# Performance work log

Hardware: AMD Instinct MI355X
Metric: run time of the kernel (lower is better)

The kernel has to match this reference:

```python
import jax, jax.numpy as jnp
import numpy as np

B, D, S, SE, H, DFF = 4, 1024, 1024, 1024, 16, 4096
DH = D // H
NUDGE = 1e-7


def norm(x):
    # x: [B, D, S]; custom layer norm: mean over (1,2), then divide by full L2 norm
    size = x.shape[1] * x.shape[2]
    mean = jnp.sum(x, axis=(1, 2)) / size
    x = x - mean[:, None, None]
    std = jnp.sqrt(jnp.sum(x * x, axis=(1, 2)))
    return x / (std[:, None, None] + NUDGE)


def mha(q_in, kv_in, Wq, Wk, Wv, Wo, causal):
    # q_in: [B, Sq, D], kv_in: [B, Sk, D]
    Bq, Sq, _ = q_in.shape
    Sk = kv_in.shape[1]
    q = (q_in @ Wq).reshape(Bq, Sq, H, DH)
    k = (kv_in @ Wk).reshape(Bq, Sk, H, DH)
    v = (kv_in @ Wv).reshape(Bq, Sk, H, DH)
    scores = jnp.einsum('bqhd,bkhd->bhqk', q, k) / jnp.sqrt(jnp.asarray(DH, q.dtype))
    if causal:
        mask = jnp.tril(jnp.ones((Sq, Sk), dtype=bool))
        scores = jnp.where(mask, scores, jnp.finfo(scores.dtype).min)
    attn = jax.nn.softmax(scores, axis=-1)
    out = jnp.einsum('bhqk,bkhd->bqhd', attn, v).reshape(Bq, Sq, D)
    return out @ Wo


def setup_inputs() -> dict:
    key = jax.random.key(0)
    ks = jax.random.split(key, 13)
    w = lambda k, sh: jax.random.normal(k, sh, dtype=jnp.float32) * 0.02
    return {
        'embedding': jax.random.normal(ks[0], (B, D, SE), dtype=jnp.float32),
        'other_inputs': jax.random.normal(ks[1], (B, D, S), dtype=jnp.float32),
        'Wq_s': w(ks[2], (D, D)), 'Wk_s': w(ks[3], (D, D)),
        'Wv_s': w(ks[4], (D, D)), 'Wo_s': w(ks[5], (D, D)),
        'Wq_c': w(ks[6], (D, D)), 'Wk_c': w(ks[7], (D, D)),
        'Wv_c': w(ks[8], (D, D)), 'Wo_c': w(ks[9], (D, D)),
        'W1': w(ks[10], (D, DFF)), 'b1': jnp.zeros((DFF,), jnp.float32),
        'W2': w(ks[11], (DFF, D)), 'b2': jnp.zeros((D,), jnp.float32),
    }


def reference(embedding, other_inputs, Wq_s, Wk_s, Wv_s, Wo_s,
              Wq_c, Wk_c, Wv_c, Wo_c, W1, b1, W2, b2):
    # tensors are [B, D, S]; attention operates on [B, S, D]
    x = other_inputs.transpose(0, 2, 1)
    sa = mha(x, x, Wq_s, Wk_s, Wv_s, Wo_s, causal=True)
    post_attention = norm(other_inputs + sa.transpose(0, 2, 1))

    pa = post_attention.transpose(0, 2, 1)
    emb = embedding.transpose(0, 2, 1)
    ca = mha(pa, emb, Wq_c, Wk_c, Wv_c, Wo_c, causal=False)
    post_embedding = norm(post_attention + ca.transpose(0, 2, 1))

    # per-token MLP (original loops over axis 2 and restacks; here fully batched)
    pe = post_embedding.transpose(0, 2, 1)  # [B, S, D]
    ff = jax.nn.relu(pe @ W1 + b1) @ W2 + b2
    return norm(post_embedding + ff.transpose(0, 2, 1))
```

## Files before the change

### kernel.cpp

```cpp
#include <hip/hip_runtime.h>
#include <cmath>

#define B_   4
#define D_   1024
#define S_   1024
#define H_   16
#define DH_  64
#define DFF_ 4096

typedef __attribute__((ext_vector_type(8))) short bf16x8;
typedef __attribute__((ext_vector_type(4))) float f32x4;

__device__ __forceinline__ unsigned short f2b(float f) {
    unsigned int u = __float_as_uint(f);
    u += 0x7fffu + ((u >> 16) & 1u);
    return (unsigned short)(u >> 16);
}

__device__ __forceinline__ void gload_lds16(const unsigned short* g, unsigned short* l) {
    __builtin_amdgcn_global_load_lds(
        (const __attribute__((address_space(1))) void*)g,
        (__attribute__((address_space(3))) void*)l, 16, 0, 0);
}

template <int BM, int BN, bool RES>
__global__ __launch_bounds__(256, 2)
void gemm_t(const unsigned short* __restrict__ A,
            const unsigned short* __restrict__ Wt,
            const float* __restrict__ bias,
            const float* __restrict__ residual,
            float* __restrict__ Cf, unsigned short* __restrict__ Cb,
            float* __restrict__ partial,
            int N, int K, int lda, int ldb, long csplit, int relu)
{
    constexpr int FM = BM / 32, FN = BN / 32;
    __shared__ unsigned short As[BM * 64];
    __shared__ unsigned short Bs[BN * 64];
    const int tid = threadIdx.x;
    const int w = tid >> 6, lane = tid & 63;
    const int quad = lane >> 4, l16 = lane & 15;
    const int m0 = blockIdx.x * BM, n0 = blockIdx.y * BN;
    const int wm = (w >> 1) * (BM / 2), wn = (w & 1) * (BN / 2);
    const int srow = lane >> 3;
    const int scol = ((lane & 7) ^ srow) * 8;

    A  += (size_t)blockIdx.z * K;
    Wt += (size_t)blockIdx.z * K;
    if (Cf) Cf += (size_t)blockIdx.z * csplit;

    f32x4 acc[FM][FN] = {};

    for (int k0 = 0; k0 < K; k0 += 64) {
#pragma unroll
        for (int i = 0; i < BM / 32; ++i) {
            const int inst = w + 4 * i;
            gload_lds16(A + (size_t)(m0 + inst * 8 + srow) * lda + k0 + scol,
                        As + inst * 512);
        }
#pragma unroll
        for (int i = 0; i < BN / 32; ++i) {
            const int inst = w + 4 * i;
            gload_lds16(Wt + (size_t)(n0 + inst * 8 + srow) * ldb + k0 + scol,
                        Bs + inst * 512);
        }
        __syncthreads();

#pragma unroll
        for (int kk = 0; kk < 2; ++kk) {
            bf16x8 af[FM], bfr[FN];
#pragma unroll
            for (int i = 0; i < FM; ++i) {
                const int r = wm + i * 16 + l16;
                af[i] = *(const bf16x8*)&As[r * 64 + (((kk * 4 + quad) ^ (r & 7)) * 8)];
            }
#pragma unroll
            for (int j = 0; j < FN; ++j) {
                const int r = wn + j * 16 + l16;
                bfr[j] = *(const bf16x8*)&Bs[r * 64 + (((kk * 4 + quad) ^ (r & 7)) * 8)];
            }
#pragma unroll
            for (int i = 0; i < FM; ++i)
#pragma unroll
                for (int j = 0; j < FN; ++j)
                    acc[i][j] = __builtin_amdgcn_mfma_f32_16x16x32_bf16(af[i], bfr[j], acc[i][j], 0, 0, 0);
        }
        __syncthreads();
    }

    float s = 0.f, ss = 0.f;
#pragma unroll
    for (int i = 0; i < FM; ++i) {
        const int grow = m0 + wm + i * 16 + quad * 4;
#pragma unroll
        for (int j = 0; j < FN; ++j) {
            const int gcol = n0 + wn + j * 16 + l16;
            const float bv = bias ? bias[gcol] : 0.f;
#pragma unroll
            for (int r = 0; r < 4; ++r) {
                float vv = acc[i][j][r] + bv;
                if (relu) vv = fmaxf(vv, 0.f);
                if constexpr (RES) {
                    vv += residual[(size_t)(grow + r) * N + gcol];
                    s += vv; ss += vv * vv;
                    Cf[(size_t)(grow + r) * N + gcol] = vv;
                } else {
                    if (Cf) Cf[(size_t)(grow + r) * N + gcol] = vv;
                    if (Cb) Cb[(size_t)(grow + r) * N + gcol] = f2b(vv);
                }
            }
        }
    }

    if constexpr (RES) {
        float* rs = (float*)As;
        float* rss = rs + 256;
        rs[tid] = s; rss[tid] = ss;
        __syncthreads();
        for (int off = 128; off > 0; off >>= 1) {
            if (tid < off) { rs[tid] += rs[tid + off]; rss[tid] += rss[tid + off]; }
            __syncthreads();
        }
        if (tid == 0) {
            constexpr int YPB = S_ / BM;
            const int b = blockIdx.x / YPB;
            const int chunk = (blockIdx.x % YPB) * gridDim.y + blockIdx.y;
            const int chunks = YPB * gridDim.y;
            partial[((size_t)b * chunks + chunk) * 2 + 0] = rs[0];
            partial[((size_t)b * chunks + chunk) * 2 + 1] = rss[0];
        }
    }
}

__global__ void reduce2_res(const float* __restrict__ pc, const float* __restrict__ res,
                            const float* __restrict__ bias, float* __restrict__ y,
                            float* __restrict__ partial)
{
    const size_t pcs = (size_t)4096 * 1024;
    const int b = blockIdx.y;
    const size_t base = (size_t)b * 1048576 + (size_t)blockIdx.x * 16384;
    float s = 0.f, ss = 0.f;
    for (int i = threadIdx.x; i < 4096; i += 256) {
        const size_t e = base + (size_t)i * 4;
        float4 v0 = *(const float4*)&pc[e];
        float4 v1 = *(const float4*)&pc[e + pcs];
        float4 rv = *(const float4*)&res[e];
        float4 bv = *(const float4*)&bias[e & 1023];
        float4 o;
        o.x = v0.x + v1.x + rv.x + bv.x;
        o.y = v0.y + v1.y + rv.y + bv.y;
        o.z = v0.z + v1.z + rv.z + bv.z;
        o.w = v0.w + v1.w + rv.w + bv.w;
        *(float4*)&y[e] = o;
        s += o.x + o.y + o.z + o.w;
        ss += o.x * o.x + o.y * o.y + o.z * o.z + o.w * o.w;
    }
    __shared__ float rs[256], rss[256];
    rs[threadIdx.x] = s; rss[threadIdx.x] = ss;
    __syncthreads();
    for (int off = 128; off > 0; off >>= 1) {
        if (threadIdx.x < off) {
            rs[threadIdx.x] += rs[threadIdx.x + off];
            rss[threadIdx.x] += rss[threadIdx.x + off];
        }
        __syncthreads();
    }
    if (threadIdx.x == 0) {
        partial[((size_t)b * 64 + blockIdx.x) * 2 + 0] = rs[0];
        partial[((size_t)b * 64 + blockIdx.x) * 2 + 1] = rss[0];
    }
}

__device__ __forceinline__ void stats_reduce(const float* __restrict__ partial,
                                             int b, int chunks, int tid,
                                             float* rs, float* rss,
                                             float& mean, float& inv)
{
    float s = 0.f, ss = 0.f;
    for (int i = tid; i < chunks; i += 256) {
        s  += partial[((size_t)b * chunks + i) * 2 + 0];
        ss += partial[((size_t)b * chunks + i) * 2 + 1];
    }
    rs[tid] = s; rss[tid] = ss;
    __syncthreads();
    for (int off = 128; off > 0; off >>= 1) {
        if (tid < off) { rs[tid] += rs[tid + off]; rss[tid] += rss[tid + off]; }
        __syncthreads();
    }
    const float size = (float)(D_ * S_);
    const float m = rs[0] / size;
    const float var = fmaxf(rss[0] - size * m * m, 0.f);
    mean = m;
    inv = 1.f / (sqrtf(var) + 1e-7f);
    __syncthreads();
}

__global__ void norm_apply_dual(float* __restrict__ y, unsigned short* __restrict__ yb,
                                const float* __restrict__ partial, int chunks)
{
    __shared__ float rs[256], rss[256];
    const int b = blockIdx.y;
    float mean, inv;
    stats_reduce(partial, b, chunks, threadIdx.x, rs, rss, mean, inv);

    const int perBatch = D_ * S_;
    float4* y4 = (float4*)(y + (size_t)b * perBatch);
    unsigned short* yb_ = yb + (size_t)b * perBatch;
    const int n4 = perBatch / 4;
    for (int i = blockIdx.x * blockDim.x + threadIdx.x; i < n4;
         i += gridDim.x * blockDim.x) {
        float4 v = y4[i];
        v.x = (v.x - mean) * inv; v.y = (v.y - mean) * inv;
        v.z = (v.z - mean) * inv; v.w = (v.w - mean) * inv;
        y4[i] = v;
        ushort4 hh; hh.x = f2b(v.x); hh.y = f2b(v.y); hh.z = f2b(v.z); hh.w = f2b(v.w);
        *(ushort4*)(yb_ + (size_t)i * 4) = hh;
    }
}

template <bool CAUSAL>
__global__ __launch_bounds__(512, 4)
void attn_mfma3(const unsigned short* __restrict__ q, const unsigned short* __restrict__ k,
                const unsigned short* __restrict__ vt, unsigned short* __restrict__ o,
                int qstride, int kstride)
{
    __shared__ unsigned short Ks[128 * 64];
    __shared__ unsigned short Vt[64 * 128];
    __shared__ unsigned short Ps[8][16][72];
    const int tid = threadIdx.x;
    const int w = tid >> 6, lane = tid & 63;
    const int quad = lane >> 4, l16 = lane & 15;
    const int h = blockIdx.y, b = blockIdx.z;
    const int qt = CAUSAL ? ((blockIdx.x + h) & 7) : blockIdx.x;
    const int q0 = qt * 128;
    const int row0 = q0 + w * 16;

    const int ksr = lane >> 3, ksc = ((lane & 7) ^ (lane >> 3)) * 8;
    const int vsr = lane >> 4, vsc = lane & 15;

    const unsigned short* qA = q + (size_t)(b * S_ + row0 + l16) * qstride + h * DH_;
    const bf16x8 qa0 = *(const bf16x8*)(qA + quad * 8);
    const bf16x8 qa1 = *(const bf16x8*)(qA + 32 + quad * 8);

    f32x4 OA[4] = {};
    float lA[4] = {};

    const int nit = CAUSAL ? (qt + 1) : (S_ / 128);
    for (int t = 0; t < nit; ++t) {
        const int j0 = t * 128;
#pragma unroll
        for (int i = 0; i < 2; ++i) {
            const int ins = w + 8 * i;
            gload_lds16(k + (size_t)(b * S_ + j0 + ins * 8 + ksr) * kstride + h * DH_ + ksc,
                        Ks + ins * 512);
            const int vrow = ins * 4 + vsr;
            gload_lds16(vt + (size_t)((b * H_ + h) * DH_ + vrow) * S_ + j0
                           + ((vsc ^ (vrow & 15)) * 8),
                        Vt + ins * 512);
        }
        __syncthreads();

#pragma unroll
        for (int g = 0; g < 2; ++g) {
            const int jg = j0 + g * 64;
            const bool doW = !CAUSAL || (jg <= row0 + 15);
            const bool needMask = CAUSAL && doW && (jg + 63 > row0);

            if (doW) {
                f32x4 stA[4];
#pragma unroll
                for (int n = 0; n < 4; ++n) {
                    const int kr = g * 64 + n * 16 + l16;
                    const bf16x8 kf0 = *(const bf16x8*)&Ks[kr * 64 + ((quad ^ (kr & 7)) * 8)];
                    const bf16x8 kf1 = *(const bf16x8*)&Ks[kr * 64 + (((quad + 4) ^ (kr & 7)) * 8)];
                    f32x4 c = {};
                    c = __builtin_amdgcn_mfma_f32_16x16x32_bf16(qa0, kf0, c, 0, 0, 0);
                    c = __builtin_amdgcn_mfma_f32_16x16x32_bf16(qa1, kf1, c, 0, 0, 0);
                    stA[n] = c;
                }

#pragma unroll
                for (int n = 0; n < 4; ++n)
#pragma unroll
                    for (int r = 0; r < 4; ++r) {
                        float sv = stA[n][r] * 0.125f;
                        if (needMask) {
                            const int row = row0 + quad * 4 + r;
                            const int key = jg + n * 16 + l16;
                            if (key > row) sv = -1e30f;
                        }
                        const float p = __expf(sv);
                        lA[r] += p;
                        Ps[w][quad * 4 + r][n * 16 + l16] = f2b(p);
                    }
                __threadfence_block();

                const bf16x8 pa0 = *(const bf16x8*)&Ps[w][l16][quad * 8];
                const bf16x8 pa1 = *(const bf16x8*)&Ps[w][l16][32 + quad * 8];
#pragma unroll
                for (int n = 0; n < 4; ++n) {
                    const int vr = n * 16 + l16;
                    const bf16x8 vf0 = *(const bf16x8*)&Vt[vr * 128 + (((g * 8 + quad) ^ l16) * 8)];
                    const bf16x8 vf1 = *(const bf16x8*)&Vt[vr * 128 + (((g * 8 + quad + 4) ^ l16) * 8)];
                    OA[n] = __builtin_amdgcn_mfma_f32_16x16x32_bf16(pa0, vf0, OA[n], 0, 0, 0);
                    OA[n] = __builtin_amdgcn_mfma_f32_16x16x32_bf16(pa1, vf1, OA[n], 0, 0, 0);
                }
            }
        }
        __syncthreads();
    }

#pragma unroll
    for (int r = 0; r < 4; ++r) {
        float la = lA[r];
        la += __shfl_xor(la, 1); la += __shfl_xor(la, 2);
        la += __shfl_xor(la, 4); la += __shfl_xor(la, 8);
        const float ia = 1.f / la;
        const size_t baseA = (size_t)(b * S_ + row0 + quad * 4 + r) * D_ + h * DH_;
#pragma unroll
        for (int n = 0; n < 4; ++n)
            o[baseA + n * 16 + l16] = f2b(OA[n][r] * ia);
    }
}

__global__ void transpose_v(const unsigned short* __restrict__ src,
                            unsigned short* __restrict__ dst, int istride)
{
    __shared__ unsigned short t[32][34];
    const int z = blockIdx.z, b = z >> 4, h = z & 15;
    const int s0 = blockIdx.x * 32, d0 = blockIdx.y * 32;
    const int tx = threadIdx.x, ty = threadIdx.y;
#pragma unroll
    for (int i = 0; i < 4; ++i)
        t[ty + i * 8][tx] =
            src[(size_t)(b * S_ + s0 + ty + i * 8) * istride + h * DH_ + d0 + tx];
    __syncthreads();
#pragma unroll
    for (int i = 0; i < 4; ++i)
        dst[(size_t)(z * DH_ + d0 + ty + i * 8) * S_ + s0 + tx] = t[tx][ty + i * 8];
}

struct WJob { const float* src; int sld; long doff; int dld; };
struct WJobs { WJob j[16]; };

__global__ void wtrans_all(WJobs js, unsigned short* __restrict__ dst)
{
    __shared__ float tile[32][33];
    const WJob J = js.j[blockIdx.z];
    const int c0 = blockIdx.x * 32, r0 = blockIdx.y * 32;
    const int tx = threadIdx.x, ty = threadIdx.y;
#pragma unroll
    for (int i = 0; i < 4; ++i)
        tile[ty + i * 8][tx] = J.src[(size_t)(r0 + ty + i * 8) * J.sld + c0 + tx];
    __syncthreads();
#pragma unroll
    for (int i = 0; i < 4; ++i)
        dst[J.doff + (size_t)(c0 + ty + i * 8) * J.dld + r0 + tx] =
            f2b(tile[tx][ty + i * 8]);
}

__global__ void transpose_in(const float* __restrict__ other, const float* __restrict__ emb,
                             float* __restrict__ f0, unsigned short* __restrict__ xb,
                             unsigned short* __restrict__ eb)
{
    __shared__ float tile[32][33];
    const int z = blockIdx.z;
    const int b = z & 3;
    const bool isEmb = z >= 4;
    const float* ip = (isEmb ? emb : other) + (size_t)b * 1048576;
    const int c0 = blockIdx.x * 32, r0 = blockIdx.y * 32;
    const int tx = threadIdx.x, ty = threadIdx.y;
#pragma unroll
    for (int i = 0; i < 4; ++i)
        tile[ty + i * 8][tx] = ip[(size_t)(r0 + ty + i * 8) * 1024 + c0 + tx];
    __syncthreads();
#pragma unroll
    for (int i = 0; i < 4; ++i) {
        const float v = tile[tx][ty + i * 8];
        const size_t oidx = (size_t)b * 1048576 + (size_t)(c0 + ty + i * 8) * 1024 + r0 + tx;
        if (isEmb) eb[oidx] = f2b(v);
        else { f0[oidx] = v; xb[oidx] = f2b(v); }
    }
}

__global__ void transpose_out(const float* __restrict__ in, float* __restrict__ outf,
                              const float* __restrict__ partial, int chunks)
{
    __shared__ float tile[32][33];
    __shared__ float rs[256], rss[256];
    const int z = blockIdx.z;
    const int tx = threadIdx.x, ty = threadIdx.y;
    const int tid = ty * 32 + tx;

    float mean, inv;
    stats_reduce(partial, z, chunks, tid, rs, rss, mean, inv);

    const float* ip = in + (size_t)z * 1048576;
    const int c0 = blockIdx.x * 32, r0 = blockIdx.y * 32;
#pragma unroll
    for (int i = 0; i < 4; ++i)
        tile[ty + i * 8][tx] = ip[(size_t)(r0 + ty + i * 8) * 1024 + c0 + tx];
    __syncthreads();
#pragma unroll
    for (int i = 0; i < 4; ++i) {
        const float v = (tile[tx][ty + i * 8] - mean) * inv;
        outf[(size_t)z * 1048576 + (size_t)(c0 + ty + i * 8) * 1024 + r0 + tx] = v;
    }
}

extern "C" void kernel_launch(void* const* d_in, const int* in_sizes, int n_in,
                              void* d_out, int out_size, void* d_ws, size_t ws_size,
                              hipStream_t stream)
{
    const float* embedding = (const float*)d_in[0];
    const float* other     = (const float*)d_in[1];
    const float* W1 = (const float*)d_in[10];
    const float* b1 = (const float*)d_in[11];
    const float* W2 = (const float*)d_in[12];
    const float* b2 = (const float*)d_in[13];
    float* out = (float*)d_out;

    char* wsb = (char*)d_ws;
    const size_t MB = 1u << 20;
    float* f0 = (float*)(wsb + 0 * MB);
    float* f2 = (float*)(wsb + 16 * MB);
    unsigned short* wts  = (unsigned short*)(wsb + 32 * MB);
    unsigned short* wqkv = wts;
    unsigned short* wo_s = wts + 3 * 1048576;
    unsigned short* wq_c = wts + 4 * 1048576;
    unsigned short* wkv_c= wts + 5 * 1048576;
    unsigned short* wo_c = wts + 7 * 1048576;
    unsigned short* w1t  = wts + 8 * 1048576;
    unsigned short* w2t  = wts + 12 * 1048576;
    unsigned short* actA = (unsigned short*)(wsb + 64 * MB);
    unsigned short* actB = (unsigned short*)(wsb + 72 * MB);
    unsigned short* actC = (unsigned short*)(wsb + 80 * MB);
    unsigned short* actC2 = actC + 4 * 1048576;
    unsigned short* aout  = actC + 12 * 1048576;
    float* pc      = (float*)(wsb + 112 * MB);
    float* partial = (float*)(wsb + 176 * MB);

    const dim3 blkT(32, 8), blk256(256), blk512(512);
    const dim3 gAttn(S_ / 128, H_, B_);
    const dim3 gVt(32, 2, B_ * H_);
    const dim3 gApply(64, B_);

    WJobs js;
    for (int z = 0; z < 8; ++z)
        js.j[z] = { (const float*)d_in[2 + z], 1024, (long)z * 1048576, 1024 };
    for (int q = 0; q < 4; ++q)
        js.j[8 + q] = { W1 + (size_t)q * 1024, 4096, (long)(8 + q) * 1048576, 1024 };
    for (int q = 0; q < 4; ++q)
        js.j[12 + q] = { W2 + (size_t)q * 1048576, 1024, 12L * 1048576 + q * 1024, 4096 };
    hipLaunchKernelGGL(wtrans_all, dim3(32, 32, 16), blkT, 0, stream, js, wts);

    hipLaunchKernelGGL(transpose_in, dim3(32, 32, 8), blkT, 0, stream,
                       other, embedding, f0, actA, actB);

    hipLaunchKernelGGL((gemm_t<128, 128, false>), dim3(32, 24), blk256, 0, stream,
                       actA, wqkv, nullptr, nullptr, nullptr, actC, nullptr,
                       3072, 1024, 1024, 1024, 0L, 0);
    hipLaunchKernelGGL(transpose_v, gVt, blkT, 0, stream, actC + 2048, actA, 3072);
    hipLaunchKernelGGL(attn_mfma3<true>, gAttn, blk512, 0, stream,
                       actC, actC + 1024, actA, aout, 3072, 3072);
    hipLaunchKernelGGL((gemm_t<64, 128, true>), dim3(64, 8), blk256, 0, stream,
                       aout, wo_s, nullptr, f0, f2, nullptr, partial,
                       1024, 1024, 1024, 1024, 0L, 0);
    hipLaunchKernelGGL(norm_apply_dual, gApply, blk256, 0, stream, f2, actA, partial, 128);

    hipLaunchKernelGGL((gemm_t<64, 128, false>), dim3(64, 8), blk256, 0, stream,
                       actA, wq_c, nullptr, nullptr, nullptr, actC, nullptr,
                       1024, 1024, 1024, 1024, 0L, 0);
    hipLaunchKernelGGL((gemm_t<128, 128, false>), dim3(32, 16), blk256, 0, stream,
                       actB, wkv_c, nullptr, nullptr, nullptr, actC2, nullptr,
                       2048, 1024, 1024, 1024, 0L, 0);
    hipLaunchKernelGGL(transpose_v, gVt, blkT, 0, stream, actC2 + 1024, actB, 2048);
    hipLaunchKernelGGL(attn_mfma3<false>, gAttn, blk512, 0, stream,
                       actC, actC2, actB, aout, 1024, 2048);
    hipLaunchKernelGGL((gemm_t<64, 128, true>), dim3(64, 8), blk256, 0, stream,
                       aout, wo_c, nullptr, f2, f0, nullptr, partial,
                       1024, 1024, 1024, 1024, 0L, 0);
    hipLaunchKernelGGL(norm_apply_dual, gApply, blk256, 0, stream, f0, actA, partial, 128);

    hipLaunchKernelGGL((gemm_t<128, 128, false>), dim3(32, 32), blk256, 0, stream,
                       actA, w1t, b1, nullptr, nullptr, actC, nullptr,
                       DFF_, 1024, 1024, 1024, 0L, 1);
    hipLaunchKernelGGL((gemm_t<128, 128, false>), dim3(32, 8, 2), blk256, 0, stream,
                       actC, w2t, nullptr, nullptr, pc, nullptr, nullptr,
                       1024, 2048, 4096, 4096, (long)4096 * 1024, 0);
    hipLaunchKernelGGL(reduce2_res, gApply, blk256, 0, stream, pc, f0, b2, f2, partial);
    hipLaunchKernelGGL(transpose_out, dim3(32, 32, B_), blkT, 0, stream, f2, out, partial, 64);

    (void)in_sizes; (void)n_in; (void)out_size; (void)ws_size;
}
```

Before: 467.7 us.

## Add 512-thread 256-row GEMM kernel with double-buffered LDS for big projections

```diff
diff --git a/kernel.cpp b/kernel.cpp
--- a/kernel.cpp
+++ b/kernel.cpp
@@ -21,6 +21,114 @@
     __builtin_amdgcn_global_load_lds(
         (const __attribute__((address_space(1))) void*)g,
         (__attribute__((address_space(3))) void*)l, 16, 0, 0);
+}
+
+template <int BN>
+__global__ __launch_bounds__(512, 2)
+void gemm8(const unsigned short* __restrict__ A,
+           const unsigned short* __restrict__ Wt,
+           const float* __restrict__ bias,
+           float* __restrict__ Cf, unsigned short* __restrict__ Cb,
+           int N, int K, int lda, int ldb, long csplit, int relu)
+{
+    constexpr int BM = 256;
+    constexpr int FM = 8, FN = BN / 64;
+    constexpr int ACALLS = BM / 64, BCALLS = BN / 64;
+    constexpr int L = ACALLS + BCALLS;
+    constexpr int ASZ = BM * 64, BSZ = BN * 64;
+    __shared__ unsigned short lds[2 * (ASZ + BSZ)];
+
+    const int tid = threadIdx.x;
+    const int w = tid >> 6, lane = tid & 63;
+    const int quad = lane >> 4, l16 = lane & 15;
+    const int m0 = blockIdx.x * BM, n0 = blockIdx.y * BN;
+    const int wm = (w >> 2) * 128;
+    const int wn = (w & 3) * (BN / 4);
+    const int srow = lane >> 3;
+    const int scol = ((lane & 7) ^ srow) * 8;
+
+    A  += (size_t)blockIdx.z * K;
+    Wt += (size_t)blockIdx.z * K;
+    if (Cf) Cf += (size_t)blockIdx.z * csplit;
+
+    const int nt = K >> 6;
+
+    auto STAGE = [&](int t, int buf) {
+        const int k0 = t << 6;
+        unsigned short* As = lds + buf * (ASZ + BSZ);
+        unsigned short* Bs = As + ASZ;
+#pragma unroll
+        for (int i = 0; i < ACALLS; ++i) {
+            const int inst = w + 8 * i;
+            gload_lds16(A + (size_t)(m0 + inst * 8 + srow) * lda + k0 + scol,
+                        As + inst * 512);
+        }
+#pragma unroll
+        for (int i = 0; i < BCALLS; ++i) {
+            const int inst = w + 8 * i;
+            gload_lds16(Wt + (size_t)(n0 + inst * 8 + srow) * ldb + k0 + scol,
+                        Bs + inst * 512);
+        }
+    };
+
+    f32x4 acc[FM][FN] = {};
+
+    STAGE(0, 0);
+    STAGE(1, 1);
+    asm volatile("s_waitcnt vmcnt(%0)\n\ts_barrier" :: "i"(L) : "memory");
+
+    int cur = 0;
+    for (int t = 0; t < nt; ++t) {
+        const unsigned short* As = lds + cur * (ASZ + BSZ);
+        const unsigned short* Bs = As + ASZ;
+#pragma unroll
+        for (int kk = 0; kk < 2; ++kk) {
+            bf16x8 af[FM], bfr[FN];
+#pragma unroll
+            for (int i = 0; i < FM; ++i) {
+                const int r = wm + i * 16 + l16;
+                af[i] = *(const bf16x8*)&As[r * 64 + (((kk * 4 + quad) ^ (r & 7)) * 8)];
+            }
+#pragma unroll
+            for (int j = 0; j < FN; ++j) {
+                const int r = wn + j * 16 + l16;
+                bfr[j] = *(const bf16x8*)&Bs[r * 64 + (((kk * 4 + quad) ^ (r & 7)) * 8)];
+            }
+            __builtin_amdgcn_s_setprio(1);
+#pragma unroll
+            for (int i = 0; i < FM; ++i)
+#pragma unroll
+                for (int j = 0; j < FN; ++j)
+                    acc[i][j] = __builtin_amdgcn_mfma_f32_16x16x32_bf16(af[i], bfr[j], acc[i][j], 0, 0, 0);
+            __builtin_amdgcn_s_setprio(0);
+        }
+        if (t == nt - 1) break;
+        asm volatile("s_barrier" ::: "memory");
+        if (t + 2 < nt) {
+            STAGE(t + 2, cur);
+            asm volatile("s_waitcnt vmcnt(%0)\n\ts_barrier" :: "i"(L) : "memory");
+        } else {
+            asm volatile("s_waitcnt vmcnt(0)\n\ts_barrier" ::: "memory");
+        }
+        cur ^= 1;
+    }
+
+#pragma unroll
+    for (int i = 0; i < FM; ++i) {
+        const int grow = m0 + wm + i * 16 + quad * 4;
+#pragma unroll
+        for (int j = 0; j < FN; ++j) {
+            const int gcol = n0 + wn + j * 16 + l16;
+            const float bv = bias ? bias[gcol] : 0.f;
+#pragma unroll
+            for (int r = 0; r < 4; ++r) {
+                float vv = acc[i][j][r] + bv;
+                if (relu) vv = fmaxf(vv, 0.f);
+                if (Cf) Cf[(size_t)(grow + r) * N + gcol] = vv;
+                if (Cb) Cb[(size_t)(grow + r) * N + gcol] = f2b(vv);
+            }
+        }
+    }
 }
 
 template <int BM, int BN, bool RES>
@@ -456,8 +564,8 @@
     hipLaunchKernelGGL(transpose_in, dim3(32, 32, 8), blkT, 0, stream,
                        other, embedding, f0, actA, actB);
 
-    hipLaunchKernelGGL((gemm_t<128, 128, false>), dim3(32, 24), blk256, 0, stream,
-                       actA, wqkv, nullptr, nullptr, nullptr, actC, nullptr,
+    hipLaunchKernelGGL((gemm8<256>), dim3(16, 12), blk512, 0, stream,
+                       actA, wqkv, nullptr, nullptr, actC,
                        3072, 1024, 1024, 1024, 0L, 0);
     hipLaunchKernelGGL(transpose_v, gVt, blkT, 0, stream, actC + 2048, actA, 3072);
     hipLaunchKernelGGL(attn_mfma3<true>, gAttn, blk512, 0, stream,
@@ -470,8 +578,8 @@
     hipLaunchKernelGGL((gemm_t<64, 128, false>), dim3(64, 8), blk256, 0, stream,
                        actA, wq_c, nullptr, nullptr, nullptr, actC, nullptr,
                        1024, 1024, 1024, 1024, 0L, 0);
-    hipLaunchKernelGGL((gemm_t<128, 128, false>), dim3(32, 16), blk256, 0, stream,
-                       actB, wkv_c, nullptr, nullptr, nullptr, actC2, nullptr,
+    hipLaunchKernelGGL((gemm8<128>), dim3(16, 16), blk512, 0, stream,
+                       actB, wkv_c, nullptr, nullptr, actC2,
                        2048, 1024, 1024, 1024, 0L, 0);
     hipLaunchKernelGGL(transpose_v, gVt, blkT, 0, stream, actC2 + 1024, actB, 2048);
     hipLaunchKernelGGL(attn_mfma3<false>, gAttn, blk512, 0, stream,
@@ -481,11 +589,11 @@
                        1024, 1024, 1024, 1024, 0L, 0);
     hipLaunchKernelGGL(norm_apply_dual, gApply, blk256, 0, stream, f0, actA, partial, 128);
 
-    hipLaunchKernelGGL((gemm_t<128, 128, false>), dim3(32, 32), blk256, 0, stream,
-                       actA, w1t, b1, nullptr, nullptr, actC, nullptr,
+    hipLaunchKernelGGL((gemm8<256>), dim3(16, 16), blk512, 0, stream,
+                       actA, w1t, b1, nullptr, actC,
                        DFF_, 1024, 1024, 1024, 0L, 1);
-    hipLaunchKernelGGL((gemm_t<128, 128, false>), dim3(32, 8, 2), blk256, 0, stream,
-                       actC, w2t, nullptr, nullptr, pc, nullptr, nullptr,
+    hipLaunchKernelGGL((gemm8<128>), dim3(16, 8, 2), blk512, 0, stream,
+                       actC, w2t, nullptr, pc, nullptr,
                        1024, 2048, 4096, 4096, (long)4096 * 1024, 0);
     hipLaunchKernelGGL(reduce2_res, gApply, blk256, 0, stream, pc, f0, b2, f2, partial);
     hipLaunchKernelGGL(transpose_out, dim3(32, 32, B_), blkT, 0, stream, f2, out, partial, 64);
```

New measurement: 478.3 us. 1.02x slower.
